# Optimization experiments

Hardware: AMD Instinct MI355X
Metric: run time of the kernel (lower is better)

Reference implementation:

```python
import jax, jax.numpy as jnp
import numpy as np

EMBED_DIM = 1024
NUM_HEADS = 16
D_K = EMBED_DIM // NUM_HEADS


def setup_inputs() -> dict:
    key = jax.random.key(0)
    ks = jax.random.split(key, 5)
    s = 1.0 / np.sqrt(EMBED_DIM)  # roughly match nn.Linear init scale
    return {
        "x": jax.random.normal(ks[0], (2, 2048, EMBED_DIM), dtype=jnp.float32),
        "wq": jax.random.normal(ks[1], (EMBED_DIM, EMBED_DIM), dtype=jnp.float32) * s,
        "wk": jax.random.normal(ks[2], (EMBED_DIM, EMBED_DIM), dtype=jnp.float32) * s,
        "wv": jax.random.normal(ks[3], (EMBED_DIM, EMBED_DIM), dtype=jnp.float32) * s,
        "wo": jax.random.normal(ks[4], (EMBED_DIM, EMBED_DIM), dtype=jnp.float32) * s,
    }


def reference(x, wq, wk, wv, wo):
    b, s, e = x.shape
    # nn.Linear(bias=False): y = x @ W.T
    def split_heads(t):
        return t.reshape(b, s, NUM_HEADS, D_K).transpose(0, 2, 1, 3)  # [b,h,s,d]
    q = split_heads(x @ wq.T)
    k = split_heads(x @ wk.T)
    v = split_heads(x @ wv.T)
    scores = jnp.einsum("bhqd,bhkd->bhqk", q, k) / jnp.sqrt(jnp.float32(D_K))
    attn = jax.nn.softmax(scores, axis=-1)
    out = jnp.einsum("bhqk,bhkd->bhqd", attn, v)  # [b,h,s,d]
    out = out.transpose(0, 2, 1, 3).reshape(b, s, e)
    return out @ wo.T
```

## Files before the change

### kernel.cpp

```cpp
#include <hip/hip_runtime.h>
#include <stdint.h>

typedef unsigned short u16;
typedef float f32x4 __attribute__((ext_vector_type(4)));
typedef __bf16 bf16x8 __attribute__((ext_vector_type(8)));
typedef short s16x4 __attribute__((ext_vector_type(4)));

__device__ __forceinline__ u16 f2bf(float f) {
  union { float f; uint32_t u; } c; c.f = f;
  uint32_t u = c.u;
  u += 0x7fffu + ((u >> 16) & 1u);
  return (u16)(u >> 16);
}

__device__ __forceinline__ uint32_t pkbf(float a, float b) {
  union { float f; uint32_t u; } ua, ub; ua.f = a; ub.f = b;
  return __builtin_amdgcn_perm(ub.u, ua.u, 0x07060302u);
}

#define GLOAD_LDS16(g, l)                                                              \
  __builtin_amdgcn_global_load_lds((__attribute__((address_space(1))) void*)(g),       \
                                   (__attribute__((address_space(3))) void*)(l), 16, 0, 0)

__global__ __launch_bounds__(256) void cvt_all(const float* __restrict__ x,
                                               const float* __restrict__ wq,
                                               const float* __restrict__ wk,
                                               const float* __restrict__ wv,
                                               const float* __restrict__ wo,
                                               u16* __restrict__ xb,
                                               u16* __restrict__ wqkvb,
                                               u16* __restrict__ wob) {
  int bx = blockIdx.x;
  const float* src;
  u16* dst;
  int i;
  if (bx < 4096) {
    src = x; dst = xb; i = bx * 256 + threadIdx.x;
  } else {
    int r = bx - 4096;
    int w = r >> 10;
    i = (r & 1023) * 256 + threadIdx.x;
    if (w == 0)      { src = wq; dst = wqkvb; }
    else if (w == 1) { src = wk; dst = wqkvb + 1048576; }
    else if (w == 2) { src = wv; dst = wqkvb + 2097152; }
    else             { src = wo; dst = wob; }
  }
  const float4 v = ((const float4*)src)[i];
  ushort4 o;
  o.x = f2bf(v.x); o.y = f2bf(v.y); o.z = f2bf(v.z); o.w = f2bf(v.w);
  ((ushort4*)dst)[i] = o;
}

__global__ __launch_bounds__(256, 3) void gemm_qkv(const u16* __restrict__ A,
                                                   const u16* __restrict__ B,
                                                   u16* __restrict__ QKb,
                                                   u16* __restrict__ Vt) {
  const int K = 1024;
  __shared__ __align__(16) u16 sA[3 * 4096];
  __shared__ __align__(16) u16 sB[3 * 4096];
  const int tid = threadIdx.x;
  const int lane = tid & 63;
  const int wave = tid >> 6;
  const int quad = lane >> 4, l16 = lane & 15;
  const int wm = (wave >> 1) * 64, wn = (wave & 1) * 64;
  const int bm = blockIdx.y * 128, bn = blockIdx.x * 128;

  f32x4 acc[4][4];
#pragma unroll
  for (int i = 0; i < 4; i++)
#pragma unroll
    for (int j = 0; j < 4; j++) acc[i][j] = (f32x4){0.f, 0.f, 0.f, 0.f};

#define QKV_STAGE(t, bi)                                                           \
  {                                                                                \
    const int k0s = (t) * 32;                                                      \
    char* dA = (char*)(sA + (bi) * 4096);                                          \
    char* dB = (char*)(sB + (bi) * 4096);                                          \
    _Pragma("unroll")                                                              \
    for (int k2 = 0; k2 < 2; k2++) {                                               \
      int u = k2 * 256 + tid;                                                      \
      int row = u >> 2, c4 = (u & 3) ^ (row & 3);                                  \
      GLOAD_LDS16(A + (size_t)(bm + row) * K + k0s + c4 * 8, dA + u * 16);         \
      GLOAD_LDS16(B + (size_t)(bn + row) * K + k0s + c4 * 8, dB + u * 16);         \
    }                                                                              \
  }

  QKV_STAGE(0, 0);
  QKV_STAGE(1, 1);

  int cur = 0, stg = 2;
  for (int T = 0; T < 32; ++T) {
    if (T < 31) asm volatile("s_waitcnt vmcnt(4)" ::: "memory");
    else        asm volatile("s_waitcnt vmcnt(0)" ::: "memory");
    __builtin_amdgcn_s_barrier();
    asm volatile("" ::: "memory");
    if (T < 30) QKV_STAGE(T + 2, stg);

    const u16* cA = sA + cur * 4096;
    const u16* cB = sB + cur * 4096;
    bf16x8 af[4], bfr[4];
#pragma unroll
    for (int mt = 0; mt < 4; mt++) {
      int ra = wm + mt * 16 + l16;
      af[mt] = *(const bf16x8*)&cA[ra * 32 + ((quad ^ (ra & 3)) * 8)];
    }
#pragma unroll
    for (int nt = 0; nt < 4; nt++) {
      int rb = wn + nt * 16 + l16;
      bfr[nt] = *(const bf16x8*)&cB[rb * 32 + ((quad ^ (rb & 3)) * 8)];
    }
#pragma unroll
    for (int mt = 0; mt < 4; mt++)
#pragma unroll
      for (int nt = 0; nt < 4; nt++)
        acc[mt][nt] = __builtin_amdgcn_mfma_f32_16x16x32_bf16(af[mt], bfr[nt], acc[mt][nt], 0, 0, 0);

    cur = (cur == 2) ? 0 : cur + 1;
    stg = (stg == 2) ? 0 : stg + 1;
  }
#undef QKV_STAGE

  if (blockIdx.x < 16) {
    const float qs = (blockIdx.x < 8) ? 0.18033688011f : 1.0f;
#pragma unroll
    for (int mt = 0; mt < 4; mt++)
#pragma unroll
      for (int nt = 0; nt < 4; nt++)
#pragma unroll
        for (int r = 0; r < 4; r++) {
          int row = bm + wm + mt * 16 + quad * 4 + r;
          int col = bn + wn + nt * 16 + l16;
          QKb[(size_t)row * 2048 + col] = f2bf(acc[mt][nt][r] * qs);
        }
  } else {
#pragma unroll
    for (int mt = 0; mt < 4; mt++)
#pragma unroll
      for (int nt = 0; nt < 4; nt++) {
        int hd = (bn - 2048) + wn + nt * 16 + l16;
        int tok = bm + wm + mt * 16 + quad * 4;
        ushort4 o;
        o.x = f2bf(acc[mt][nt][0]);
        o.y = f2bf(acc[mt][nt][1]);
        o.z = f2bf(acc[mt][nt][2]);
        o.w = f2bf(acc[mt][nt][3]);
        *(ushort4*)&Vt[(size_t)hd * 4096 + tok] = o;
      }
  }
}

__global__ __launch_bounds__(512, 4) void attn_fwd(const u16* __restrict__ QKb,
                                                   const u16* __restrict__ Vt,
                                                   u16* __restrict__ O) {
  const int bx = blockIdx.x;
  const int qt = bx >> 5;
  const int h  = (bx >> 1) & 15;
  const int b  = bx & 1;
  const int tid = threadIdx.x;
  const int lane = tid & 63;
  const int wave = tid >> 6;
  const int wq = wave >> 1;
  const int wk = wave & 1;
  const int quad = lane >> 4, l16 = lane & 15;

  __shared__ __align__(16) u16 smem[32768];
  u16* sQ = smem;
  u16* sK = smem + 8192;
  u16* sV = smem + 20480;

  const int tok0 = b * 2048;
  const int q0 = qt * 128;
  const int colh = h * 64;

#pragma unroll
  for (int k2 = 0; k2 < 2; k2++) {
    int c = k2 * 512 + tid;
    int row = c >> 3, c8 = (c & 7) ^ (row & 7);
    GLOAD_LDS16(QKb + (size_t)(tok0 + q0 + row) * 2048 + colh + c8 * 8,
                (char*)sQ + c * 16);
  }
#pragma unroll
  for (int t = 0; t < 2; t++) {
    int c = tid;
    int row = c >> 3, c8 = (c & 7) ^ (row & 7);
    GLOAD_LDS16(QKb + (size_t)(tok0 + t * 64 + row) * 2048 + 1024 + colh + c8 * 8,
                (char*)(sK + t * 4096) + c * 16);
    GLOAD_LDS16(Vt + (size_t)(colh + row) * 4096 + tok0 + t * 64 + c8 * 8,
                (char*)(sV + t * 4096) + c * 16);
  }
  asm volatile("s_waitcnt vmcnt(4)" ::: "memory");
  __builtin_amdgcn_s_barrier();
  asm volatile("" ::: "memory");

  bf16x8 aq[2][2];
#pragma unroll
  for (int sub = 0; sub < 2; sub++)
#pragma unroll
    for (int kh = 0; kh < 2; kh++) {
      int rq = wq * 32 + sub * 16 + l16;
      aq[sub][kh] = *(const bf16x8*)&sQ[rq * 64 + (((kh * 4 + quad) ^ (rq & 7)) * 8)];
    }

  f32x4 oacc[2][4];
  float lsum[2];
#pragma unroll
  for (int sub = 0; sub < 2; sub++) {
    lsum[sub] = 0.f;
#pragma unroll
    for (int db = 0; db < 4; db++) oacc[sub][db] = (f32x4){0.f, 0.f, 0.f, 0.f};
  }

  int cur = 0, stg = 2;
  for (int it = 0; it < 32; ++it) {
    if (it < 31) asm volatile("s_waitcnt vmcnt(2)" ::: "memory");
    else         asm volatile("s_waitcnt vmcnt(0)" ::: "memory");
    __builtin_amdgcn_s_barrier();
    asm volatile("" ::: "memory");
    if (it < 30) {
      const int nkv = (it + 2) * 64;
      int c = tid;
      int row = c >> 3, c8 = (c & 7) ^ (row & 7);
      GLOAD_LDS16(QKb + (size_t)(tok0 + nkv + row) * 2048 + 1024 + colh + c8 * 8,
                  (char*)(sK + stg * 4096) + c * 16);
      GLOAD_LDS16(Vt + (size_t)(colh + row) * 4096 + tok0 + nkv + c8 * 8,
                  (char*)(sV + stg * 4096) + c * 16);
    }
    const u16* sKc = sK + cur * 4096;
    const u16* sVc = sV + cur * 4096;

    bf16x8 kf[2][2];
#pragma unroll
    for (int nt = 0; nt < 2; nt++)
#pragma unroll
      for (int kh = 0; kh < 2; kh++) {
        int rr = wk * 32 + nt * 16 + l16;
        kf[nt][kh] = *(const bf16x8*)&sKc[rr * 64 + (((kh * 4 + quad) ^ (rr & 7)) * 8)];
      }
    s16x4 vf[4][2];
#pragma unroll
    for (int db = 0; db < 4; db++)
#pragma unroll
      for (int nt = 0; nt < 2; nt++) {
        int row = db * 16 + l16;
        int c16 = ((wk * 2 + nt) * 2 + (quad >> 1)) ^ (row & 7);
        vf[db][nt] = *(const s16x4*)&sVc[row * 64 + c16 * 8 + (quad & 1) * 4];
      }

#pragma unroll
    for (int sub = 0; sub < 2; sub++) {
#pragma unroll
      for (int nt = 0; nt < 2; nt++) {
        f32x4 c = (f32x4){0.f, 0.f, 0.f, 0.f};
        c = __builtin_amdgcn_mfma_f32_16x16x32_bf16(kf[nt][0], aq[sub][0], c, 0, 0, 0);
        c = __builtin_amdgcn_mfma_f32_16x16x32_bf16(kf[nt][1], aq[sub][1], c, 0, 0, 0);
        float e0 = __builtin_amdgcn_exp2f(c[0]);
        float e1 = __builtin_amdgcn_exp2f(c[1]);
        float e2 = __builtin_amdgcn_exp2f(c[2]);
        float e3 = __builtin_amdgcn_exp2f(c[3]);
        lsum[sub] += (e0 + e1) + (e2 + e3);
        union { uint32_t u[2]; s16x4 v; } bb;
        bb.u[0] = pkbf(e0, e1);
        bb.u[1] = pkbf(e2, e3);
#pragma unroll
        for (int db = 0; db < 4; db++)
          oacc[sub][db] = __builtin_amdgcn_mfma_f32_16x16x16bf16_1k(vf[db][nt], bb.v, oacc[sub][db], 0, 0, 0);
      }
    }
    cur = (cur == 2) ? 0 : cur + 1;
    stg = (stg == 2) ? 0 : stg + 1;
  }

  asm volatile("s_waitcnt lgkmcnt(0)" ::: "memory");
  __builtin_amdgcn_s_barrier();

#pragma unroll
  for (int sub = 0; sub < 2; sub++) {
    float v = lsum[sub];
    v += __shfl_xor(v, 16, 64);
    v += __shfl_xor(v, 32, 64);
    lsum[sub] = v;
  }

  float* Rbase = (float*)smem + wq * 2048;
  float* lsumT = (float*)((char*)smem + 32768);

  if (wk == 0) {
#pragma unroll
    for (int sub = 0; sub < 2; sub++) {
#pragma unroll
      for (int db = 0; db < 4; db++) {
        int q = sub * 16 + l16;
        int d = db * 16 + quad * 4;
        *(f32x4*)&Rbase[q * 64 + (d ^ ((q & 7) << 3))] = oacc[sub][db];
      }
      if (quad == 0) lsumT[wq * 32 + sub * 16 + l16] = lsum[sub];
    }
  }
  __builtin_amdgcn_s_barrier();
  if (wk == 1) {
#pragma unroll
    for (int sub = 0; sub < 2; sub++) {
      int q = sub * 16 + l16;
      float rt = 1.0f / (lsum[sub] + lsumT[wq * 32 + q]);
#pragma unroll
      for (int db = 0; db < 4; db++) {
        int d = db * 16 + quad * 4;
        f32x4 o = *(const f32x4*)&Rbase[q * 64 + (d ^ ((q & 7) << 3))] + oacc[sub][db];
        ushort4 st;
        st.x = f2bf(o[0] * rt);
        st.y = f2bf(o[1] * rt);
        st.z = f2bf(o[2] * rt);
        st.w = f2bf(o[3] * rt);
        *(ushort4*)&O[(size_t)(tok0 + q0 + wq * 32 + q) * 1024 + colh + d] = st;
      }
    }
  }
}

__global__ __launch_bounds__(256) void gemm_out(const u16* __restrict__ A,
                                                const u16* __restrict__ B,
                                                float* __restrict__ C) {
  const int N = 1024, K = 1024;
  __shared__ __align__(16) u16 sA[3 * 4096];
  __shared__ __align__(16) u16 sB[3 * 2048];
  const int tid = threadIdx.x;
  const int lane = tid & 63;
  const int wave = tid >> 6;
  const int quad = lane >> 4, l16 = lane & 15;
  const int wm = (wave >> 1) * 64, wn = (wave & 1) * 32;
  const int bm = blockIdx.y * 128, bn = blockIdx.x * 64;

  f32x4 acc[4][2];
#pragma unroll
  for (int i = 0; i < 4; i++)
#pragma unroll
    for (int j = 0; j < 2; j++) acc[i][j] = (f32x4){0.f, 0.f, 0.f, 0.f};

#define OUT_STAGE(t, bi)                                                           \
  {                                                                                \
    const int k0s = (t) * 32;                                                      \
    char* dA = (char*)(sA + (bi) * 4096);                                          \
    char* dB = (char*)(sB + (bi) * 2048);                                          \
    _Pragma("unroll")                                                              \
    for (int k2 = 0; k2 < 2; k2++) {                                               \
      int u = k2 * 256 + tid;                                                      \
      int row = u >> 2, c4 = (u & 3) ^ (row & 3);                                  \
      GLOAD_LDS16(A + (size_t)(bm + row) * K + k0s + c4 * 8, dA + u * 16);         \
    }                                                                              \
    {                                                                              \
      int u = tid;                                                                 \
      int row = u >> 2, c4 = (u & 3) ^ (row & 3);                                  \
      GLOAD_LDS16(B + (size_t)(bn + row) * K + k0s + c4 * 8, dB + u * 16);         \
    }                                                                              \
  }

  OUT_STAGE(0, 0);
  OUT_STAGE(1, 1);

  int cur = 0, stg = 2;
  for (int T = 0; T < 32; ++T) {
    if (T < 31) asm volatile("s_waitcnt vmcnt(3)" ::: "memory");
    else        asm volatile("s_waitcnt vmcnt(0)" ::: "memory");
    __builtin_amdgcn_s_barrier();
    asm volatile("" ::: "memory");
    if (T < 30) OUT_STAGE(T + 2, stg);

    const u16* cA = sA + cur * 4096;
    const u16* cB = sB + cur * 2048;
    bf16x8 af[4], bfr[2];
#pragma unroll
    for (int mt = 0; mt < 4; mt++) {
      int ra = wm + mt * 16 + l16;
      af[mt] = *(const bf16x8*)&cA[ra * 32 + ((quad ^ (ra & 3)) * 8)];
    }
#pragma unroll
    for (int nt = 0; nt < 2; nt++) {
      int rb = wn + nt * 16 + l16;
      bfr[nt] = *(const bf16x8*)&cB[rb * 32 + ((quad ^ (rb & 3)) * 8)];
    }
#pragma unroll
    for (int mt = 0; mt < 4; mt++)
#pragma unroll
      for (int nt = 0; nt < 2; nt++)
        acc[mt][nt] = __builtin_amdgcn_mfma_f32_16x16x32_bf16(af[mt], bfr[nt], acc[mt][nt], 0, 0, 0);

    cur = (cur == 2) ? 0 : cur + 1;
    stg = (stg == 2) ? 0 : stg + 1;
  }
#undef OUT_STAGE

#pragma unroll
  for (int mt = 0; mt < 4; mt++)
#pragma unroll
    for (int nt = 0; nt < 2; nt++)
#pragma unroll
      for (int r = 0; r < 4; r++) {
        int row = bm + wm + mt * 16 + quad * 4 + r;
        int col = bn + wn + nt * 16 + l16;
        C[(size_t)row * N + col] = acc[mt][nt][r];
      }
}

extern "C" void kernel_launch(void* const* d_in, const int* in_sizes, int n_in,
                              void* d_out, int out_size, void* d_ws, size_t ws_size,
                              hipStream_t stream) {
  const float* x  = (const float*)d_in[0];
  const float* wq = (const float*)d_in[1];
  const float* wk = (const float*)d_in[2];
  const float* wv = (const float*)d_in[3];
  const float* wo = (const float*)d_in[4];
  float* out = (float*)d_out;
  char* ws = (char*)d_ws;
  const size_t MB = 1u << 20;

  u16* xb    = (u16*)(ws);
  u16* wqkvb = (u16*)(ws + 8 * MB);
  u16* wob   = (u16*)(ws + 14 * MB);
  u16* QKb   = (u16*)(ws + 16 * MB);
  u16* Vtb   = (u16*)(ws + 32 * MB);
  u16* Ob    = xb;

  cvt_all<<<8192, 256, 0, stream>>>(x, wq, wk, wv, wo, xb, wqkvb, wob);

  gemm_qkv<<<dim3(24, 32), 256, 0, stream>>>(xb, wqkvb, QKb, Vtb);

  attn_fwd<<<512, 512, 0, stream>>>(QKb, Vtb, Ob);

  gemm_out<<<dim3(16, 32), 256, 0, stream>>>(Ob, wob, out);
}
```

Before: 180.0 us.

## Software-pipeline QK^T of next tile with softmax and PV of previous tile

Restructures the attention inner loop so the QK^T MFMAs for iteration i+1 are issued before the exp/PV work of iteration i, using ping-pong score registers. V gets a 4-slot ring in LDS (enlarged shared memory) so the V tile stays live one extra iteration. The aim is to overlap MFMA score computation with transcendental exp and PV MFMAs and hide LDS latency. The cost is higher register and LDS pressure, which could lower occupancy under launch_bounds(512,4), plus an added lgkmcnt wait at each barrier.

```diff
diff --git a/kernel.cpp b/kernel.cpp
--- a/kernel.cpp
+++ b/kernel.cpp
@@ -163,7 +163,7 @@
   const int wk = wave & 1;
   const int quad = lane >> 4, l16 = lane & 15;
 
-  __shared__ __align__(16) u16 smem[32768];
+  __shared__ __align__(16) u16 smem[36864];
   u16* sQ = smem;
   u16* sK = smem + 8192;
   u16* sV = smem + 20480;
@@ -210,65 +210,88 @@
     for (int db = 0; db < 4; db++) oacc[sub][db] = (f32x4){0.f, 0.f, 0.f, 0.f};
   }
 
-  int cur = 0, stg = 2;
-  for (int it = 0; it < 32; ++it) {
-    if (it < 31) asm volatile("s_waitcnt vmcnt(2)" ::: "memory");
-    else         asm volatile("s_waitcnt vmcnt(0)" ::: "memory");
-    __builtin_amdgcn_s_barrier();
-    asm volatile("" ::: "memory");
-    if (it < 30) {
-      const int nkv = (it + 2) * 64;
-      int c = tid;
-      int row = c >> 3, c8 = (c & 7) ^ (row & 7);
-      GLOAD_LDS16(QKb + (size_t)(tok0 + nkv + row) * 2048 + 1024 + colh + c8 * 8,
-                  (char*)(sK + stg * 4096) + c * 16);
-      GLOAD_LDS16(Vt + (size_t)(colh + row) * 4096 + tok0 + nkv + c8 * 8,
-                  (char*)(sV + stg * 4096) + c * 16);
-    }
-    const u16* sKc = sK + cur * 4096;
-    const u16* sVc = sV + cur * 4096;
-
-    bf16x8 kf[2][2];
-#pragma unroll
-    for (int nt = 0; nt < 2; nt++)
-#pragma unroll
-      for (int kh = 0; kh < 2; kh++) {
-        int rr = wk * 32 + nt * 16 + l16;
-        kf[nt][kh] = *(const bf16x8*)&sKc[rr * 64 + (((kh * 4 + quad) ^ (rr & 7)) * 8)];
-      }
-    s16x4 vf[4][2];
-#pragma unroll
-    for (int db = 0; db < 4; db++)
-#pragma unroll
-      for (int nt = 0; nt < 2; nt++) {
-        int row = db * 16 + l16;
-        int c16 = ((wk * 2 + nt) * 2 + (quad >> 1)) ^ (row & 7);
-        vf[db][nt] = *(const s16x4*)&sVc[row * 64 + c16 * 8 + (quad & 1) * 4];
-      }
-
-#pragma unroll
-    for (int sub = 0; sub < 2; sub++) {
-#pragma unroll
-      for (int nt = 0; nt < 2; nt++) {
-        f32x4 c = (f32x4){0.f, 0.f, 0.f, 0.f};
-        c = __builtin_amdgcn_mfma_f32_16x16x32_bf16(kf[nt][0], aq[sub][0], c, 0, 0, 0);
-        c = __builtin_amdgcn_mfma_f32_16x16x32_bf16(kf[nt][1], aq[sub][1], c, 0, 0, 0);
-        float e0 = __builtin_amdgcn_exp2f(c[0]);
-        float e1 = __builtin_amdgcn_exp2f(c[1]);
-        float e2 = __builtin_amdgcn_exp2f(c[2]);
-        float e3 = __builtin_amdgcn_exp2f(c[3]);
-        lsum[sub] += (e0 + e1) + (e2 + e3);
-        union { uint32_t u[2]; s16x4 v; } bb;
-        bb.u[0] = pkbf(e0, e1);
-        bb.u[1] = pkbf(e2, e3);
-#pragma unroll
-        for (int db = 0; db < 4; db++)
-          oacc[sub][db] = __builtin_amdgcn_mfma_f32_16x16x16bf16_1k(vf[db][nt], bb.v, oacc[sub][db], 0, 0, 0);
-      }
-    }
-    cur = (cur == 2) ? 0 : cur + 1;
-    stg = (stg == 2) ? 0 : stg + 1;
-  }
+  int kc = 0, stg3 = 2;
+
+#define ITER_LOAD(IT, SS)                                                            \
+  {                                                                                  \
+    asm volatile("s_waitcnt lgkmcnt(0)" ::: "memory");                               \
+    if ((IT) < 31) asm volatile("s_waitcnt vmcnt(2)" ::: "memory");                  \
+    else           asm volatile("s_waitcnt vmcnt(0)" ::: "memory");                  \
+    __builtin_amdgcn_s_barrier();                                                    \
+    asm volatile("" ::: "memory");                                                   \
+    if ((IT) < 30) {                                                                 \
+      const int nkv = ((IT) + 2) * 64;                                               \
+      int c = tid;                                                                   \
+      int row = c >> 3, c8 = (c & 7) ^ (row & 7);                                    \
+      GLOAD_LDS16(QKb + (size_t)(tok0 + nkv + row) * 2048 + 1024 + colh + c8 * 8,    \
+                  (char*)(sK + stg3 * 4096) + c * 16);                               \
+      GLOAD_LDS16(Vt + (size_t)(colh + row) * 4096 + tok0 + nkv + c8 * 8,            \
+                  (char*)(sV + (((IT) + 2) & 3) * 4096) + c * 16);                   \
+    }                                                                                \
+    const u16* sKc = sK + kc * 4096;                                                 \
+    bf16x8 kf[2][2];                                                                 \
+    _Pragma("unroll")                                                                \
+    for (int nt = 0; nt < 2; nt++)                                                   \
+      _Pragma("unroll")                                                              \
+      for (int kh = 0; kh < 2; kh++) {                                               \
+        int rr = wk * 32 + nt * 16 + l16;                                            \
+        kf[nt][kh] = *(const bf16x8*)&sKc[rr * 64 + (((kh * 4 + quad) ^ (rr & 7)) * 8)]; \
+      }                                                                              \
+    _Pragma("unroll")                                                                \
+    for (int sub = 0; sub < 2; sub++)                                                \
+      _Pragma("unroll")                                                              \
+      for (int nt = 0; nt < 2; nt++) {                                               \
+        f32x4 c0 = (f32x4){0.f, 0.f, 0.f, 0.f};                                      \
+        c0 = __builtin_amdgcn_mfma_f32_16x16x32_bf16(kf[nt][0], aq[sub][0], c0, 0, 0, 0); \
+        SS[sub][nt] = __builtin_amdgcn_mfma_f32_16x16x32_bf16(kf[nt][1], aq[sub][1], c0, 0, 0, 0); \
+      }                                                                              \
+    kc = (kc == 2) ? 0 : kc + 1;                                                     \
+    stg3 = (stg3 == 2) ? 0 : stg3 + 1;                                               \
+  }
+
+#define ITER_SOFT(TT, SS)                                                            \
+  {                                                                                  \
+    const u16* sVp = sV + ((TT) & 3) * 4096;                                         \
+    _Pragma("unroll")                                                                \
+    for (int nt = 0; nt < 2; nt++) {                                                 \
+      s16x4 vf[4];                                                                   \
+      _Pragma("unroll")                                                              \
+      for (int db = 0; db < 4; db++) {                                               \
+        int row = db * 16 + l16;                                                     \
+        int c16 = ((wk * 2 + nt) * 2 + (quad >> 1)) ^ (row & 7);                     \
+        vf[db] = *(const s16x4*)&sVp[row * 64 + c16 * 8 + (quad & 1) * 4];           \
+      }                                                                              \
+      _Pragma("unroll")                                                              \
+      for (int sub = 0; sub < 2; sub++) {                                            \
+        f32x4 cS = SS[sub][nt];                                                      \
+        float e0 = __builtin_amdgcn_exp2f(cS[0]);                                    \
+        float e1 = __builtin_amdgcn_exp2f(cS[1]);                                    \
+        float e2 = __builtin_amdgcn_exp2f(cS[2]);                                    \
+        float e3 = __builtin_amdgcn_exp2f(cS[3]);                                    \
+        lsum[sub] += (e0 + e1) + (e2 + e3);                                          \
+        union { uint32_t u[2]; s16x4 v; } bb;                                        \
+        bb.u[0] = pkbf(e0, e1);                                                      \
+        bb.u[1] = pkbf(e2, e3);                                                      \
+        _Pragma("unroll")                                                            \
+        for (int db = 0; db < 4; db++)                                               \
+          oacc[sub][db] = __builtin_amdgcn_mfma_f32_16x16x16bf16_1k(vf[db], bb.v, oacc[sub][db], 0, 0, 0); \
+      }                                                                              \
+    }                                                                                \
+  }
+
+  f32x4 SA[2][2], SB[2][2];
+  ITER_LOAD(0, SA);
+  for (int it = 1; it < 31; it += 2) {
+    ITER_LOAD(it, SB);
+    ITER_SOFT(it - 1, SA);
+    ITER_LOAD(it + 1, SA);
+    ITER_SOFT(it, SB);
+  }
+  ITER_LOAD(31, SB);
+  ITER_SOFT(30, SA);
+  ITER_SOFT(31, SB);
+#undef ITER_LOAD
+#undef ITER_SOFT
 
   asm volatile("s_waitcnt lgkmcnt(0)" ::: "memory");
   __builtin_amdgcn_s_barrier();
```

Measured after the change: 179.8 us. About the same (-0.1%).
